# Kernel tuning notes

Hardware: AMD Instinct MI355X
Metric: run time of the kernel (lower is better)

## Reference

```python
import jax, jax.numpy as jnp
import numpy as np

NEG_SLOPE = 0.2  # negative_slope of LeakyReLU in GATConv
N_NODES = 50000
N_EDGES = 800000
R = 2
IN_DIM = 128
HID = 32
HEADS = 4
OUT = 32


def setup_inputs() -> dict:
    key = jax.random.key(0)
    ks = jax.random.split(key, 12)
    s = 0.1  # keep pre-activations tame
    x = jax.random.normal(ks[0], (N_NODES, IN_DIM), dtype=jnp.float32)
    W1 = jax.random.normal(ks[1], (R, IN_DIM, HEADS * HID), dtype=jnp.float32) * s
    al1 = jax.random.normal(ks[2], (R, HEADS, HID), dtype=jnp.float32) * s
    ar1 = jax.random.normal(ks[3], (R, HEADS, HID), dtype=jnp.float32) * s
    b1 = jax.random.normal(ks[4], (R, HEADS * HID), dtype=jnp.float32) * s
    W2 = jax.random.normal(ks[5], (R, HEADS * HID, HEADS * OUT), dtype=jnp.float32) * s
    al2 = jax.random.normal(ks[6], (R, HEADS, OUT), dtype=jnp.float32) * s
    ar2 = jax.random.normal(ks[7], (R, HEADS, OUT), dtype=jnp.float32) * s
    b2 = jax.random.normal(ks[8], (R, HEADS * OUT), dtype=jnp.float32) * s
    edges = jax.random.randint(ks[9], (R, 2, N_EDGES), 0, N_NODES, dtype=jnp.int32)
    return {"x": x, "W1": W1, "al1": al1, "ar1": ar1, "b1": b1,
            "W2": W2, "al2": al2, "ar2": ar2, "b2": b2, "edges": edges}


def _gat_rel(h, W, al, ar, src, dst, n):
    """Single-relation GATConv aggregation (no bias/residual/activation)."""
    H, D = al.shape
    feat = (h @ W).reshape(n, H, D)                   # [N,H,D]
    el = jnp.einsum('nhd,hd->nh', feat, al)           # [N,H]
    er = jnp.einsum('nhd,hd->nh', feat, ar)
    e = el[src] + er[dst]                             # [E,H]
    e = jnp.where(e > 0, e, NEG_SLOPE * e)            # LeakyReLU
    # edge softmax over incoming edges of each dst node (numerically stable)
    m = jax.ops.segment_max(e, dst, num_segments=n)
    ex = jnp.exp(e - m[dst])
    denom = jax.ops.segment_sum(ex, dst, num_segments=n)
    alpha = ex / jnp.maximum(denom[dst], 1e-9)        # [E,H]
    msg = alpha[:, :, None] * feat[src]               # [E,H,D]
    return jax.ops.segment_sum(msg, dst, num_segments=n)  # [N,H,D]


def reference(x, W1, al1, ar1, b1, W2, al2, ar2, b2, edges):
    n = x.shape[0]
    r_count = edges.shape[0]
    H1, D1 = al1.shape[1:]
    # --- layer 1: per-relation GATConv (bias + elu inside), sum across relations
    acc = jnp.zeros((n, H1, D1), dtype=x.dtype)
    for r in range(r_count):
        src, dst = edges[r, 0], edges[r, 1]
        o = _gat_rel(x, W1[r], al1[r], ar1[r], src, dst, n)
        acc = acc + jax.nn.elu(o + b1[r].reshape(1, H1, D1))
    h = acc.reshape(n, H1 * D1)                       # flatten heads
    # --- layer 2: residual (identity, since in == heads*out), bias, no activation
    H2, D2 = al2.shape[1:]
    res = h.reshape(n, H2, D2)
    acc2 = jnp.zeros((n, H2, D2), dtype=x.dtype)
    for r in range(r_count):
        src, dst = edges[r, 0], edges[r, 1]
        o = _gat_rel(h, W2[r], al2[r], ar2[r], src, dst, n)
        acc2 = acc2 + o + res + b2[r].reshape(1, H2, D2)
    return acc2.mean(axis=1)                          # mean over heads -> [N, OUT]
```

## Files before the change

### kernel.cpp

```cpp
#include <hip/hip_runtime.h>
#include <math.h>

#define HEADS 4
#define DIM 32
#define FDIM 128
#define EPB 8192
#define BPBSH 8
#define WB 16

typedef __attribute__((ext_vector_type(8))) short short8;
typedef __attribute__((ext_vector_type(16))) float float16;

__device__ __forceinline__ unsigned short f2bf(float x) {
  unsigned u = __float_as_uint(x);
  u += 0x7FFFu + ((u >> 16) & 1);
  return (unsigned short)(u >> 16);
}

__global__ __launch_bounds__(256) void binA_kernel(const int* __restrict__ edges,
    int* __restrict__ cntA, const float* __restrict__ W1, const float* __restrict__ W2,
    unsigned short* __restrict__ WT, int E, int BA, int BAp, int R) {
  int r = blockIdx.y, blk = blockIdx.x, t = threadIdx.x;
  if (blk >= BA) {
    int wb = blk - BA;
    int base = wb * (32768 / WB);
#pragma unroll
    for (int j = 0; j < 32768 / WB; j += 256) {
      int idx = base + j + t;
      int layer = idx >> 14;
      int rem = idx & 16383;
      int n = rem >> 7, k = rem & 127;
      const float* W = layer ? (W2 + (size_t)r * FDIM * FDIM)
                             : (W1 + (size_t)r * FDIM * FDIM);
      WT[((size_t)(layer * R + r) << 14) + rem] = f2bf(W[k * FDIM + n]);
    }
    return;
  }
  __shared__ int hist[256];
  hist[t] = 0;
  __syncthreads();
  const int* dst = edges + (size_t)r * 2 * E + E;
  int base = blk * EPB;
#pragma unroll
  for (int j = 0; j < EPB / 256; ++j) {
    int e = base + t + j * 256;
    if (e < E) atomicAdd(&hist[dst[e] >> BPBSH], 1);
  }
  __syncthreads();
  cntA[((size_t)r * 256 + t) * BAp + blk] = hist[t];
}

__global__ __launch_bounds__(256) void scanA_kernel(int* __restrict__ cntA,
    int* __restrict__ bucketBase, int E, int NB, int BA, int BAp) {
  __shared__ int stot[256];
  int r = blockIdx.x, b = threadIdx.x;
  int* row = cntA + ((size_t)r * 256 + b) * BAp;
  int tot = 0;
  if (b < NB)
    for (int blk = 0; blk < BA; ++blk) tot += row[blk];
  stot[b] = tot;
  __syncthreads();
  for (int ofs = 1; ofs < 256; ofs <<= 1) {
    int u = (b >= ofs) ? stot[b - ofs] : 0;
    __syncthreads();
    stot[b] += u;
    __syncthreads();
  }
  int excl = stot[b] - tot;
  if (b < NB) bucketBase[r * 257 + b] = excl;
  if (b == 0) bucketBase[r * 257 + NB] = E;
  if (b < NB) {
    int run = excl;
    for (int blk = 0; blk < BA; ++blk) {
      int c = row[blk];
      row[blk] = run;
      run += c;
    }
  }
}

__global__ __launch_bounds__(256) void scatterA_kernel(const int* __restrict__ edges,
    const int* __restrict__ cntA, unsigned* __restrict__ binned, int E, int BA, int BAp) {
  __shared__ int cur[256];
  int r = blockIdx.y, blk = blockIdx.x, t = threadIdx.x;
  cur[t] = cntA[((size_t)r * 256 + t) * BAp + blk];
  __syncthreads();
  const int* srcp = edges + (size_t)r * 2 * E;
  const int* dstp = srcp + E;
  unsigned* bout = binned + (size_t)r * E;
  int base = blk * EPB;
#pragma unroll
  for (int j = 0; j < EPB / 256; ++j) {
    int e = base + t + j * 256;
    if (e < E) {
      int d = dstp[e], s = srcp[e];
      int pos = atomicAdd(&cur[d >> BPBSH], 1);
      bout[pos] = ((unsigned)d << 16) | (unsigned)s;
    }
  }
}

__global__ __launch_bounds__(256) void passB_kernel(const unsigned* __restrict__ binned,
    const int* __restrict__ bucketBase, int* __restrict__ csr, int* __restrict__ indptr,
    int E, int N, int NB) {
  __shared__ int cnt[256];
  __shared__ int off[256];
  __shared__ int cur[256];
  int r = blockIdx.y, b = blockIdx.x, t = threadIdx.x;
  int beg = bucketBase[r * 257 + b];
  int end = bucketBase[r * 257 + b + 1];
  cnt[t] = 0;
  __syncthreads();
  const unsigned* bin = binned + (size_t)r * E;
  for (int i = beg + t; i < end; i += 256)
    atomicAdd(&cnt[(bin[i] >> 16) & 255], 1);
  __syncthreads();
  for (int ofs = 1; ofs < 256; ofs <<= 1) {
    int u = (t >= ofs) ? cnt[t - ofs] : 0;
    __syncthreads();
    cnt[t] += u;
    __syncthreads();
  }
  int ex = beg + ((t > 0) ? cnt[t - 1] : 0);
  off[t] = ex;
  cur[t] = ex;
  __syncthreads();
  int node = b * 256 + t;
  if (node < N) indptr[(size_t)r * (N + 1) + node] = off[t];
  if (b == NB - 1 && t == 0) indptr[(size_t)r * (N + 1) + N] = E;
  int* csr_r = csr + (size_t)r * E;
  for (int i = beg + t; i < end; i += 256) {
    unsigned p = bin[i];
    int rank = atomicAdd(&cur[(p >> 16) & 255], 1);
    csr_r[rank] = (int)(p & 0xFFFFu);
  }
}

__global__ __launch_bounds__(256) void mm_kernel(const float* __restrict__ A,
    const unsigned short* __restrict__ WTl, const float* __restrict__ al_all,
    const float* __restrict__ ar_all, unsigned short* __restrict__ featb_all,
    float* __restrict__ el_all, float* __restrict__ er_all, int N) {
  __shared__ unsigned short sA[128 * 136];
  __shared__ float sAl[FDIM], sAr[FDIM];
  int r = blockIdx.y;
  const unsigned short* WT = WTl + (size_t)r * FDIM * FDIM;
  int row0 = blockIdx.x * 128;
  int t = threadIdx.x;
  if (t < FDIM) {
    sAl[t] = al_all[r * FDIM + t];
    sAr[t] = ar_all[r * FDIM + t];
  }
#pragma unroll
  for (int it = 0; it < 16; ++it) {
    int idx = t * 4 + it * 1024;
    int row = idx >> 7, k = idx & 127;
    int grow = row0 + row;
    float4 v = make_float4(0.f, 0.f, 0.f, 0.f);
    if (grow < N) v = *(const float4*)(A + (size_t)grow * FDIM + k);
    unsigned short* p = sA + row * 136 + k;
    p[0] = f2bf(v.x); p[1] = f2bf(v.y); p[2] = f2bf(v.z); p[3] = f2bf(v.w);
  }
  __syncthreads();
  int lane = t & 63, w = t >> 6;
  int m = lane & 31, q = lane >> 5;
  float16 acc[4] = {0.f, 0.f, 0.f, 0.f};
#pragma unroll
  for (int kc = 0; kc < 8; ++kc) {
    int ko = kc * 16 + q * 8;
    short8 a = *(const short8*)(sA + (w * 32 + m) * 136 + ko);
#pragma unroll
    for (int nt = 0; nt < 4; ++nt) {
      short8 bb = *(const short8*)(WT + (size_t)(nt * 32 + m) * FDIM + ko);
      acc[nt] = __builtin_amdgcn_mfma_f32_32x32x16_bf16(a, bb, acc[nt], 0, 0, 0);
    }
  }
  __syncthreads();
#pragma unroll
  for (int nt = 0; nt < 4; ++nt) {
#pragma unroll
    for (int reg = 0; reg < 16; ++reg) {
      int rr = (reg & 3) + 8 * (reg >> 2) + 4 * q;
      sA[(w * 32 + rr) * 136 + nt * 32 + m] = f2bf(acc[nt][reg]);
    }
  }
  __syncthreads();
  unsigned short* fb = featb_all + (size_t)r * N * FDIM;
#pragma unroll
  for (int it = 0; it < 8; ++it) {
    int idx = (t + it * 256) * 8;
    int row = idx >> 7, k = idx & 127;
    int grow = row0 + row;
    if (grow < N)
      *(uint4*)(fb + (size_t)grow * FDIM + k) = *(const uint4*)(sA + row * 136 + k);
  }
  int rowc = t >> 1, grow = row0 + rowc;
  if (grow < N) {
    float* elr = el_all + (size_t)r * N * 4;
    float* err_ = er_all + (size_t)r * N * 4;
#pragma unroll
    for (int hh = 0; hh < 2; ++hh) {
      int hd = (t & 1) * 2 + hh;
      const uint4* rp4 = (const uint4*)(sA + rowc * 136 + hd * DIM);
      const float4* alp = (const float4*)(sAl + hd * DIM);
      const float4* arp = (const float4*)(sAr + hd * DIM);
      float sl = 0.f, sr = 0.f;
#pragma unroll
      for (int gq = 0; gq < 4; ++gq) {
        uint4 u = rp4[gq];
        float4 a0 = alp[2 * gq], a1 = alp[2 * gq + 1];
        float4 r0 = arp[2 * gq], r1 = arp[2 * gq + 1];
        unsigned uv[4] = {u.x, u.y, u.z, u.w};
        float fv[8];
#pragma unroll
        for (int j = 0; j < 4; ++j) {
          fv[2 * j] = __uint_as_float(uv[j] << 16);
          fv[2 * j + 1] = __uint_as_float(uv[j] & 0xFFFF0000u);
        }
        sl = fmaf(fv[0], a0.x, sl); sr = fmaf(fv[0], r0.x, sr);
        sl = fmaf(fv[1], a0.y, sl); sr = fmaf(fv[1], r0.y, sr);
        sl = fmaf(fv[2], a0.z, sl); sr = fmaf(fv[2], r0.z, sr);
        sl = fmaf(fv[3], a0.w, sl); sr = fmaf(fv[3], r0.w, sr);
        sl = fmaf(fv[4], a1.x, sl); sr = fmaf(fv[4], r1.x, sr);
        sl = fmaf(fv[5], a1.y, sl); sr = fmaf(fv[5], r1.y, sr);
        sl = fmaf(fv[6], a1.z, sl); sr = fmaf(fv[6], r1.z, sr);
        sl = fmaf(fv[7], a1.w, sl); sr = fmaf(fv[7], r1.w, sr);
      }
      elr[(size_t)grow * 4 + hd] = sl;
      err_[(size_t)grow * 4 + hd] = sr;
    }
  }
}

__global__ __launch_bounds__(256) void agg1_kernel(const unsigned short* __restrict__ featb,
    const float* __restrict__ el, const float* __restrict__ er,
    const int* __restrict__ indptr, const int* __restrict__ csr,
    const float* __restrict__ bias, float* __restrict__ hout, int N, int E, int R) {
  int t = blockIdx.x * 256 + threadIdx.x;
  int node = t >> 3;
  if (node >= N) return;
  int hd = t & 3, sub = (t >> 2) & 1;
  float tot[32];
#pragma unroll
  for (int i = 0; i < 32; ++i) tot[i] = 0.f;
  for (int r = 0; r < R; ++r) {
    const unsigned short* f = featb + (size_t)r * N * FDIM + hd * DIM;
    const float* elr = el + (size_t)r * N * 4;
    const int* csr_r = csr + (size_t)r * E;
    const int* ip = indptr + (size_t)r * (N + 1);
    float er_h = er[(size_t)r * N * 4 + node * 4 + hd];
    int beg = ip[node], end = ip[node + 1];
    float l = 0.f, a[32];
#pragma unroll
    for (int i = 0; i < 32; ++i) a[i] = 0.f;
    for (int i = beg + sub; i < end; i += 2) {
      int s = csr_r[i];
      float ee = elr[s * 4 + hd] + er_h;
      ee = ee > 0.f ? ee : 0.2f * ee;
      float p = __expf(ee);
      const uint4* fp = (const uint4*)(f + (size_t)s * FDIM);
      uint4 u0 = fp[0], u1 = fp[1], u2 = fp[2], u3 = fp[3];
      l += p;
      unsigned uu[16] = {u0.x, u0.y, u0.z, u0.w, u1.x, u1.y, u1.z, u1.w,
                         u2.x, u2.y, u2.z, u2.w, u3.x, u3.y, u3.z, u3.w};
#pragma unroll
      for (int j = 0; j < 16; ++j) {
        float f0 = __uint_as_float(uu[j] << 16);
        float f1 = __uint_as_float(uu[j] & 0xFFFF0000u);
        a[2 * j]     = fmaf(p, f0, a[2 * j]);
        a[2 * j + 1] = fmaf(p, f1, a[2 * j + 1]);
      }
    }
    l += __shfl_xor(l, 4);
#pragma unroll
    for (int i = 0; i < 32; ++i) a[i] += __shfl_xor(a[i], 4);
    float inv = (l > 0.f) ? 1.f / l : 0.f;
    const float4* b4 = (const float4*)(bias + r * FDIM + hd * DIM);
#pragma unroll
    for (int g = 0; g < 8; ++g) {
      float4 bv = b4[g];
      float v0 = a[4 * g] * inv + bv.x;
      float v1 = a[4 * g + 1] * inv + bv.y;
      float v2 = a[4 * g + 2] * inv + bv.z;
      float v3 = a[4 * g + 3] * inv + bv.w;
      tot[4 * g]     += v0 > 0.f ? v0 : __expf(v0) - 1.f;
      tot[4 * g + 1] += v1 > 0.f ? v1 : __expf(v1) - 1.f;
      tot[4 * g + 2] += v2 > 0.f ? v2 : __expf(v2) - 1.f;
      tot[4 * g + 3] += v3 > 0.f ? v3 : __expf(v3) - 1.f;
    }
  }
  if (sub == 0) {
    float4* hp = (float4*)(hout + (size_t)node * FDIM + hd * DIM);
#pragma unroll
    for (int g = 0; g < 8; ++g)
      hp[g] = make_float4(tot[4 * g], tot[4 * g + 1], tot[4 * g + 2], tot[4 * g + 3]);
  }
}

__global__ __launch_bounds__(256) void agg2_kernel(const unsigned short* __restrict__ featb,
    const float* __restrict__ el, const float* __restrict__ er,
    const int* __restrict__ indptr, const int* __restrict__ csr,
    const float* __restrict__ bias, const float* __restrict__ hf,
    float* __restrict__ out, int N, int E, int R) {
  int t = blockIdx.x * 256 + threadIdx.x;
  int node = t >> 3;
  if (node >= N) return;
  int hd = t & 3, sub = (t >> 2) & 1;
  float tot[32];
#pragma unroll
  for (int i = 0; i < 32; ++i) tot[i] = 0.f;
  for (int r = 0; r < R; ++r) {
    const unsigned short* f = featb + (size_t)r * N * FDIM + hd * DIM;
    const float* elr = el + (size_t)r * N * 4;
    const int* csr_r = csr + (size_t)r * E;
    const int* ip = indptr + (size_t)r * (N + 1);
    float er_h = er[(size_t)r * N * 4 + node * 4 + hd];
    int beg = ip[node], end = ip[node + 1];
    float l = 0.f, a[32];
#pragma unroll
    for (int i = 0; i < 32; ++i) a[i] = 0.f;
    for (int i = beg + sub; i < end; i += 2) {
      int s = csr_r[i];
      float ee = elr[s * 4 + hd] + er_h;
      ee = ee > 0.f ? ee : 0.2f * ee;
      float p = __expf(ee);
      const uint4* fp = (const uint4*)(f + (size_t)s * FDIM);
      uint4 u0 = fp[0], u1 = fp[1], u2 = fp[2], u3 = fp[3];
      l += p;
      unsigned uu[16] = {u0.x, u0.y, u0.z, u0.w, u1.x, u1.y, u1.z, u1.w,
                         u2.x, u2.y, u2.z, u2.w, u3.x, u3.y, u3.z, u3.w};
#pragma unroll
      for (int j = 0; j < 16; ++j) {
        float f0 = __uint_as_float(uu[j] << 16);
        float f1 = __uint_as_float(uu[j] & 0xFFFF0000u);
        a[2 * j]     = fmaf(p, f0, a[2 * j]);
        a[2 * j + 1] = fmaf(p, f1, a[2 * j + 1]);
      }
    }
    l += __shfl_xor(l, 4);
#pragma unroll
    for (int i = 0; i < 32; ++i) a[i] += __shfl_xor(a[i], 4);
    float inv = (l > 0.f) ? 1.f / l : 0.f;
    const float4* b4 = (const float4*)(bias + r * FDIM + hd * DIM);
#pragma unroll
    for (int g = 0; g < 8; ++g) {
      float4 bv = b4[g];
      tot[4 * g]     += a[4 * g] * inv + bv.x;
      tot[4 * g + 1] += a[4 * g + 1] * inv + bv.y;
      tot[4 * g + 2] += a[4 * g + 2] * inv + bv.z;
      tot[4 * g + 3] += a[4 * g + 3] * inv + bv.w;
    }
  }
  {
    const float4* rv4 = (const float4*)(hf + (size_t)node * FDIM + hd * DIM);
#pragma unroll
    for (int g = 0; g < 8; ++g) {
      float4 rv = rv4[g];
      tot[4 * g]     += R * rv.x;
      tot[4 * g + 1] += R * rv.y;
      tot[4 * g + 2] += R * rv.z;
      tot[4 * g + 3] += R * rv.w;
    }
  }
#pragma unroll
  for (int i = 0; i < 32; ++i) {
    float v = tot[i];
    v += __shfl_xor(v, 1);
    v += __shfl_xor(v, 2);
    tot[i] = v * 0.25f;
  }
  if (sub == 0) {
    float4* op = (float4*)(out + (size_t)node * 32 + hd * 8);
    op[0] = make_float4(tot[hd * 8], tot[hd * 8 + 1], tot[hd * 8 + 2], tot[hd * 8 + 3]);
    op[1] = make_float4(tot[hd * 8 + 4], tot[hd * 8 + 5], tot[hd * 8 + 6], tot[hd * 8 + 7]);
  }
}

extern "C" void kernel_launch(void* const* d_in, const int* in_sizes, int n_in,
                              void* d_out, int out_size, void* d_ws, size_t ws_size,
                              hipStream_t stream) {
  const float* x   = (const float*)d_in[0];
  const float* W1  = (const float*)d_in[1];
  const float* al1 = (const float*)d_in[2];
  const float* ar1 = (const float*)d_in[3];
  const float* b1  = (const float*)d_in[4];
  const float* W2  = (const float*)d_in[5];
  const float* al2 = (const float*)d_in[6];
  const float* ar2 = (const float*)d_in[7];
  const float* b2  = (const float*)d_in[8];
  const int* edges = (const int*)d_in[9];
  float* out = (float*)d_out;

  const int N = in_sizes[0] / FDIM;
  const int R = in_sizes[1] / (FDIM * FDIM);
  const int E = in_sizes[9] / (2 * R);
  const int BA = (E + EPB - 1) / EPB;
  const int BAp = (BA + 3) & ~3;
  const int NB = (N + 255) >> BPBSH;

  char* ws = (char*)d_ws;
  size_t off = 0;
  auto alloc = [&](size_t bytes) {
    char* p = ws + off;
    off += (bytes + 255) & ~(size_t)255;
    return p;
  };
  unsigned short* featb = (unsigned short*)alloc((size_t)R * N * FDIM * 2);
  unsigned short* WT    = (unsigned short*)alloc((size_t)2 * R * FDIM * FDIM * 2);
  float* el = (float*)alloc((size_t)R * N * 4 * 4);
  float* er = (float*)alloc((size_t)R * N * 4 * 4);
  float* h  = (float*)alloc((size_t)N * FDIM * 4);
  int* cntA = (int*)alloc((size_t)R * 256 * BAp * 4);
  int* bucketBase = (int*)alloc((size_t)R * 257 * 4);
  unsigned* binned = (unsigned*)alloc((size_t)R * E * 4);
  int* csr = (int*)alloc((size_t)R * E * 4);
  int* indptr = (int*)alloc((size_t)R * (N + 1) * 4);

  dim3 bgrid(BA + WB, R);
  binA_kernel<<<bgrid, 256, 0, stream>>>(edges, cntA, W1, W2, WT, E, BA, BAp, R);
  scanA_kernel<<<R, 256, 0, stream>>>(cntA, bucketBase, E, NB, BA, BAp);
  dim3 sgrid(BA, R);
  scatterA_kernel<<<sgrid, 256, 0, stream>>>(edges, cntA, binned, E, BA, BAp);
  dim3 pgrid(NB, R);
  passB_kernel<<<pgrid, 256, 0, stream>>>(binned, bucketBase, csr, indptr, E, N, NB);

  dim3 mmgrid((N + 127) / 128, R);
  int agrid = (N * 8 + 255) / 256;

  mm_kernel<<<mmgrid, 256, 0, stream>>>(x, WT, al1, ar1, featb, el, er, N);
  agg1_kernel<<<agrid, 256, 0, stream>>>(featb, el, er, indptr, csr, b1, h, N, E, R);

  mm_kernel<<<mmgrid, 256, 0, stream>>>(h, WT + (size_t)R * FDIM * FDIM, al2, ar2, featb, el, er, N);
  agg2_kernel<<<agrid, 256, 0, stream>>>(featb, el, er, indptr, csr, b2, h, out, N, E, R);
}
```

Before: 369.1 us.

## Split aggregation across relations per thread group and unroll edge loop by two

The aggregation kernels now give each node 16 threads instead of 8, so the two relations are processed in parallel by separate lane groups and summed with an extra cross-lane shuffle. The edge loop is unrolled to issue two neighbors' gathers before accumulating, and launch bounds request 4 blocks per CU. The aim is more memory-level parallelism for the latency-bound gathers. The cost is twice as many threads, extra shuffles, and possible register pressure from the doubled in-flight loads.

```diff
diff --git a/kernel.cpp b/kernel.cpp
--- a/kernel.cpp
+++ b/kernel.cpp
@@ -231,18 +231,31 @@
   }
 }
 
-__global__ __launch_bounds__(256) void agg1_kernel(const unsigned short* __restrict__ featb,
+__device__ __forceinline__ void acc_edge(float (&a)[32], uint4 u0, uint4 u1,
+                                         uint4 u2, uint4 u3, float p) {
+  unsigned uu[16] = {u0.x, u0.y, u0.z, u0.w, u1.x, u1.y, u1.z, u1.w,
+                     u2.x, u2.y, u2.z, u2.w, u3.x, u3.y, u3.z, u3.w};
+#pragma unroll
+  for (int j = 0; j < 16; ++j) {
+    float f0 = __uint_as_float(uu[j] << 16);
+    float f1 = __uint_as_float(uu[j] & 0xFFFF0000u);
+    a[2 * j]     = fmaf(p, f0, a[2 * j]);
+    a[2 * j + 1] = fmaf(p, f1, a[2 * j + 1]);
+  }
+}
+
+__global__ __launch_bounds__(256, 4) void agg1_kernel(const unsigned short* __restrict__ featb,
     const float* __restrict__ el, const float* __restrict__ er,
     const int* __restrict__ indptr, const int* __restrict__ csr,
     const float* __restrict__ bias, float* __restrict__ hout, int N, int E, int R) {
   int t = blockIdx.x * 256 + threadIdx.x;
-  int node = t >> 3;
+  int node = t >> 4;
   if (node >= N) return;
-  int hd = t & 3, sub = (t >> 2) & 1;
+  int hd = t & 3, rr = (t >> 2) & 1, sub = (t >> 3) & 1;
   float tot[32];
 #pragma unroll
   for (int i = 0; i < 32; ++i) tot[i] = 0.f;
-  for (int r = 0; r < R; ++r) {
+  for (int r = rr; r < R; r += 2) {
     const unsigned short* f = featb + (size_t)r * N * FDIM + hd * DIM;
     const float* elr = el + (size_t)r * N * 4;
     const int* csr_r = csr + (size_t)r * E;
@@ -252,27 +265,35 @@
     float l = 0.f, a[32];
 #pragma unroll
     for (int i = 0; i < 32; ++i) a[i] = 0.f;
-    for (int i = beg + sub; i < end; i += 2) {
+    int i = beg + sub;
+    for (; i + 2 < end; i += 4) {
+      int s0 = csr_r[i], s1 = csr_r[i + 2];
+      const uint4* fp0 = (const uint4*)(f + (size_t)s0 * FDIM);
+      const uint4* fp1 = (const uint4*)(f + (size_t)s1 * FDIM);
+      float ee0 = elr[s0 * 4 + hd];
+      float ee1 = elr[s1 * 4 + hd];
+      uint4 u00 = fp0[0], u01 = fp0[1], u02 = fp0[2], u03 = fp0[3];
+      uint4 u10 = fp1[0], u11 = fp1[1], u12 = fp1[2], u13 = fp1[3];
+      ee0 += er_h; ee0 = ee0 > 0.f ? ee0 : 0.2f * ee0;
+      ee1 += er_h; ee1 = ee1 > 0.f ? ee1 : 0.2f * ee1;
+      float p0 = __expf(ee0), p1 = __expf(ee1);
+      l += p0 + p1;
+      acc_edge(a, u00, u01, u02, u03, p0);
+      acc_edge(a, u10, u11, u12, u13, p1);
+    }
+    if (i < end) {
       int s = csr_r[i];
+      const uint4* fp = (const uint4*)(f + (size_t)s * FDIM);
       float ee = elr[s * 4 + hd] + er_h;
+      uint4 u0 = fp[0], u1 = fp[1], u2 = fp[2], u3 = fp[3];
       ee = ee > 0.f ? ee : 0.2f * ee;
       float p = __expf(ee);
-      const uint4* fp = (const uint4*)(f + (size_t)s * FDIM);
-      uint4 u0 = fp[0], u1 = fp[1], u2 = fp[2], u3 = fp[3];
       l += p;
-      unsigned uu[16] = {u0.x, u0.y, u0.z, u0.w, u1.x, u1.y, u1.z, u1.w,
-                         u2.x, u2.y, u2.z, u2.w, u3.x, u3.y, u3.z, u3.w};
-#pragma unroll
-      for (int j = 0; j < 16; ++j) {
-        float f0 = __uint_as_float(uu[j] << 16);
-        float f1 = __uint_as_float(uu[j] & 0xFFFF0000u);
-        a[2 * j]     = fmaf(p, f0, a[2 * j]);
-        a[2 * j + 1] = fmaf(p, f1, a[2 * j + 1]);
-      }
-    }
-    l += __shfl_xor(l, 4);
-#pragma unroll
-    for (int i = 0; i < 32; ++i) a[i] += __shfl_xor(a[i], 4);
+      acc_edge(a, u0, u1, u2, u3, p);
+    }
+    l += __shfl_xor(l, 8);
+#pragma unroll
+    for (int k = 0; k < 32; ++k) a[k] += __shfl_xor(a[k], 8);
     float inv = (l > 0.f) ? 1.f / l : 0.f;
     const float4* b4 = (const float4*)(bias + r * FDIM + hd * DIM);
 #pragma unroll
@@ -288,7 +309,9 @@
       tot[4 * g + 3] += v3 > 0.f ? v3 : __expf(v3) - 1.f;
     }
   }
-  if (sub == 0) {
+#pragma unroll
+  for (int k = 0; k < 32; ++k) tot[k] += __shfl_xor(tot[k], 4);
+  if ((t & 12) == 0) {
     float4* hp = (float4*)(hout + (size_t)node * FDIM + hd * DIM);
 #pragma unroll
     for (int g = 0; g < 8; ++g)
@@ -296,19 +319,19 @@
   }
 }
 
-__global__ __launch_bounds__(256) void agg2_kernel(const unsigned short* __restrict__ featb,
+__global__ __launch_bounds__(256, 4) void agg2_kernel(const unsigned short* __restrict__ featb,
     const float* __restrict__ el, const float* __restrict__ er,
     const int* __restrict__ indptr, const int* __restrict__ csr,
     const float* __restrict__ bias, const float* __restrict__ hf,
     float* __restrict__ out, int N, int E, int R) {
   int t = blockIdx.x * 256 + threadIdx.x;
-  int node = t >> 3;
+  int node = t >> 4;
   if (node >= N) return;
-  int hd = t & 3, sub = (t >> 2) & 1;
+  int hd = t & 3, rr = (t >> 2) & 1, sub = (t >> 3) & 1;
   float tot[32];
 #pragma unroll
   for (int i = 0; i < 32; ++i) tot[i] = 0.f;
-  for (int r = 0; r < R; ++r) {
+  for (int r = rr; r < R; r += 2) {
     const unsigned short* f = featb + (size_t)r * N * FDIM + hd * DIM;
     const float* elr = el + (size_t)r * N * 4;
     const int* csr_r = csr + (size_t)r * E;
@@ -318,27 +341,35 @@
     float l = 0.f, a[32];
 #pragma unroll
     for (int i = 0; i < 32; ++i) a[i] = 0.f;
-    for (int i = beg + sub; i < end; i += 2) {
+    int i = beg + sub;
+    for (; i + 2 < end; i += 4) {
+      int s0 = csr_r[i], s1 = csr_r[i + 2];
+      const uint4* fp0 = (const uint4*)(f + (size_t)s0 * FDIM);
+      const uint4* fp1 = (const uint4*)(f + (size_t)s1 * FDIM);
+      float ee0 = elr[s0 * 4 + hd];
+      float ee1 = elr[s1 * 4 + hd];
+      uint4 u00 = fp0[0], u01 = fp0[1], u02 = fp0[2], u03 = fp0[3];
+      uint4 u10 = fp1[0], u11 = fp1[1], u12 = fp1[2], u13 = fp1[3];
+      ee0 += er_h; ee0 = ee0 > 0.f ? ee0 : 0.2f * ee0;
+      ee1 += er_h; ee1 = ee1 > 0.f ? ee1 : 0.2f * ee1;
+      float p0 = __expf(ee0), p1 = __expf(ee1);
+      l += p0 + p1;
+      acc_edge(a, u00, u01, u02, u03, p0);
+      acc_edge(a, u10, u11, u12, u13, p1);
+    }
+    if (i < end) {
       int s = csr_r[i];
+      const uint4* fp = (const uint4*)(f + (size_t)s * FDIM);
       float ee = elr[s * 4 + hd] + er_h;
+      uint4 u0 = fp[0], u1 = fp[1], u2 = fp[2], u3 = fp[3];
       ee = ee > 0.f ? ee : 0.2f * ee;
       float p = __expf(ee);
-      const uint4* fp = (const uint4*)(f + (size_t)s * FDIM);
-      uint4 u0 = fp[0], u1 = fp[1], u2 = fp[2], u3 = fp[3];
       l += p;
-      unsigned uu[16] = {u0.x, u0.y, u0.z, u0.w, u1.x, u1.y, u1.z, u1.w,
-                         u2.x, u2.y, u2.z, u2.w, u3.x, u3.y, u3.z, u3.w};
-#pragma unroll
-      for (int j = 0; j < 16; ++j) {
-        float f0 = __uint_as_float(uu[j] << 16);
-        float f1 = __uint_as_float(uu[j] & 0xFFFF0000u);
-        a[2 * j]     = fmaf(p, f0, a[2 * j]);
-        a[2 * j + 1] = fmaf(p, f1, a[2 * j + 1]);
-      }
-    }
-    l += __shfl_xor(l, 4);
-#pragma unroll
-    for (int i = 0; i < 32; ++i) a[i] += __shfl_xor(a[i], 4);
+      acc_edge(a, u0, u1, u2, u3, p);
+    }
+    l += __shfl_xor(l, 8);
+#pragma unroll
+    for (int k = 0; k < 32; ++k) a[k] += __shfl_xor(a[k], 8);
     float inv = (l > 0.f) ? 1.f / l : 0.f;
     const float4* b4 = (const float4*)(bias + r * FDIM + hd * DIM);
 #pragma unroll
@@ -350,6 +381,8 @@
       tot[4 * g + 3] += a[4 * g + 3] * inv + bv.w;
     }
   }
+#pragma unroll
+  for (int k = 0; k < 32; ++k) tot[k] += __shfl_xor(tot[k], 4);
   {
     const float4* rv4 = (const float4*)(hf + (size_t)node * FDIM + hd * DIM);
 #pragma unroll
@@ -368,7 +401,7 @@
     v += __shfl_xor(v, 2);
     tot[i] = v * 0.25f;
   }
-  if (sub == 0) {
+  if ((t & 12) == 0) {
     float4* op = (float4*)(out + (size_t)node * 32 + hd * 8);
     op[0] = make_float4(tot[hd * 8], tot[hd * 8 + 1], tot[hd * 8 + 2], tot[hd * 8 + 3]);
     op[1] = make_float4(tot[hd * 8 + 4], tot[hd * 8 + 5], tot[hd * 8 + 6], tot[hd * 8 + 7]);
@@ -424,7 +457,7 @@
   passB_kernel<<<pgrid, 256, 0, stream>>>(binned, bucketBase, csr, indptr, E, N, NB);
 
   dim3 mmgrid((N + 127) / 128, R);
-  int agrid = (N * 8 + 255) / 256;
+  int agrid = (N * 16 + 255) / 256;
 
   mm_kernel<<<mmgrid, 256, 0, stream>>>(x, WT, al1, ar1, featb, el, er, N);
   agg1_kernel<<<agrid, 256, 0, stream>>>(featb, el, er, indptr, csr, b1, h, N, E, R);
```

Measured after the change: 439.7 us. 19.1% more time.

## Sort nodes by degree for aggregation load balance and shrink CSR to 16-bit

Applied to the files above, without the earlier changes.

Adds a counting sort of nodes by total in-degree, in descending order: a histogram, a scan and a scatter build a permutation. The aggregation kernels then walk nodes in that order, so wavefronts hold nodes of similar degree and do less divergent looping. The CSR source indices are also stored as 16-bit shorts instead of ints, halving the index traffic. The sort adds four small launches, and the output and feature accesses per wavefront become scattered rather than contiguous. The 16-bit indices rely on node ids fitting in 16 bits, which already held in the packed binning format.

```diff
diff --git a/kernel.cpp b/kernel.cpp
--- a/kernel.cpp
+++ b/kernel.cpp
@@ -101,8 +101,8 @@
 }
 
 __global__ __launch_bounds__(256) void passB_kernel(const unsigned* __restrict__ binned,
-    const int* __restrict__ bucketBase, int* __restrict__ csr, int* __restrict__ indptr,
-    int E, int N, int NB) {
+    const int* __restrict__ bucketBase, unsigned short* __restrict__ csr,
+    int* __restrict__ indptr, int E, int N, int NB) {
   __shared__ int cnt[256];
   __shared__ int off[256];
   __shared__ int cur[256];
@@ -128,12 +128,54 @@
   int node = b * 256 + t;
   if (node < N) indptr[(size_t)r * (N + 1) + node] = off[t];
   if (b == NB - 1 && t == 0) indptr[(size_t)r * (N + 1) + N] = E;
-  int* csr_r = csr + (size_t)r * E;
+  unsigned short* csr_r = csr + (size_t)r * E;
   for (int i = beg + t; i < end; i += 256) {
     unsigned p = bin[i];
     int rank = atomicAdd(&cur[(p >> 16) & 255], 1);
-    csr_r[rank] = (int)(p & 0xFFFFu);
-  }
+    csr_r[rank] = (unsigned short)(p & 0xFFFFu);
+  }
+}
+
+__global__ __launch_bounds__(256) void degZero_kernel(int* __restrict__ dhist) {
+  dhist[threadIdx.x] = 0;
+}
+
+__global__ __launch_bounds__(256) void degHist_kernel(const int* __restrict__ indptr,
+    int* __restrict__ dhist, int N, int R) {
+  int n = blockIdx.x * 256 + threadIdx.x;
+  if (n >= N) return;
+  int d = 0;
+  for (int r = 0; r < R; ++r)
+    d += indptr[(size_t)r * (N + 1) + n + 1] - indptr[(size_t)r * (N + 1) + n];
+  if (d > 255) d = 255;
+  atomicAdd(&dhist[d], 1);
+}
+
+__global__ __launch_bounds__(256) void degScan_kernel(const int* __restrict__ dhist,
+    int* __restrict__ dcur) {
+  __shared__ int s[256];
+  int t = threadIdx.x;
+  s[t] = dhist[255 - t];
+  __syncthreads();
+  for (int ofs = 1; ofs < 256; ofs <<= 1) {
+    int u = (t >= ofs) ? s[t - ofs] : 0;
+    __syncthreads();
+    s[t] += u;
+    __syncthreads();
+  }
+  dcur[255 - t] = s[t] - dhist[255 - t];
+}
+
+__global__ __launch_bounds__(256) void degScatter_kernel(const int* __restrict__ indptr,
+    int* __restrict__ dcur, int* __restrict__ perm, int N, int R) {
+  int n = blockIdx.x * 256 + threadIdx.x;
+  if (n >= N) return;
+  int d = 0;
+  for (int r = 0; r < R; ++r)
+    d += indptr[(size_t)r * (N + 1) + n + 1] - indptr[(size_t)r * (N + 1) + n];
+  if (d > 255) d = 255;
+  int pos = atomicAdd(&dcur[d], 1);
+  perm[pos] = n;
 }
 
 __global__ __launch_bounds__(256) void mm_kernel(const float* __restrict__ A,
@@ -233,11 +275,13 @@
 
 __global__ __launch_bounds__(256) void agg1_kernel(const unsigned short* __restrict__ featb,
     const float* __restrict__ el, const float* __restrict__ er,
-    const int* __restrict__ indptr, const int* __restrict__ csr,
+    const int* __restrict__ indptr, const unsigned short* __restrict__ csr,
+    const int* __restrict__ perm,
     const float* __restrict__ bias, float* __restrict__ hout, int N, int E, int R) {
   int t = blockIdx.x * 256 + threadIdx.x;
-  int node = t >> 3;
-  if (node >= N) return;
+  int ni = t >> 3;
+  if (ni >= N) return;
+  int node = perm[ni];
   int hd = t & 3, sub = (t >> 2) & 1;
   float tot[32];
 #pragma unroll
@@ -245,7 +289,7 @@
   for (int r = 0; r < R; ++r) {
     const unsigned short* f = featb + (size_t)r * N * FDIM + hd * DIM;
     const float* elr = el + (size_t)r * N * 4;
-    const int* csr_r = csr + (size_t)r * E;
+    const unsigned short* csr_r = csr + (size_t)r * E;
     const int* ip = indptr + (size_t)r * (N + 1);
     float er_h = er[(size_t)r * N * 4 + node * 4 + hd];
     int beg = ip[node], end = ip[node + 1];
@@ -298,12 +342,14 @@
 
 __global__ __launch_bounds__(256) void agg2_kernel(const unsigned short* __restrict__ featb,
     const float* __restrict__ el, const float* __restrict__ er,
-    const int* __restrict__ indptr, const int* __restrict__ csr,
+    const int* __restrict__ indptr, const unsigned short* __restrict__ csr,
+    const int* __restrict__ perm,
     const float* __restrict__ bias, const float* __restrict__ hf,
     float* __restrict__ out, int N, int E, int R) {
   int t = blockIdx.x * 256 + threadIdx.x;
-  int node = t >> 3;
-  if (node >= N) return;
+  int ni = t >> 3;
+  if (ni >= N) return;
+  int node = perm[ni];
   int hd = t & 3, sub = (t >> 2) & 1;
   float tot[32];
 #pragma unroll
@@ -311,7 +357,7 @@
   for (int r = 0; r < R; ++r) {
     const unsigned short* f = featb + (size_t)r * N * FDIM + hd * DIM;
     const float* elr = el + (size_t)r * N * 4;
-    const int* csr_r = csr + (size_t)r * E;
+    const unsigned short* csr_r = csr + (size_t)r * E;
     const int* ip = indptr + (size_t)r * (N + 1);
     float er_h = er[(size_t)r * N * 4 + node * 4 + hd];
     int beg = ip[node], end = ip[node + 1];
@@ -412,8 +458,11 @@
   int* cntA = (int*)alloc((size_t)R * 256 * BAp * 4);
   int* bucketBase = (int*)alloc((size_t)R * 257 * 4);
   unsigned* binned = (unsigned*)alloc((size_t)R * E * 4);
-  int* csr = (int*)alloc((size_t)R * E * 4);
+  unsigned short* csr = (unsigned short*)alloc((size_t)R * E * 2);
   int* indptr = (int*)alloc((size_t)R * (N + 1) * 4);
+  int* dhist = (int*)alloc(256 * 4);
+  int* dcur  = (int*)alloc(256 * 4);
+  int* perm  = (int*)alloc((size_t)N * 4);
 
   dim3 bgrid(BA + WB, R);
   binA_kernel<<<bgrid, 256, 0, stream>>>(edges, cntA, W1, W2, WT, E, BA, BAp, R);
@@ -423,12 +472,18 @@
   dim3 pgrid(NB, R);
   passB_kernel<<<pgrid, 256, 0, stream>>>(binned, bucketBase, csr, indptr, E, N, NB);
 
+  int ngrid = (N + 255) / 256;
+  degZero_kernel<<<1, 256, 0, stream>>>(dhist);
+  degHist_kernel<<<ngrid, 256, 0, stream>>>(indptr, dhist, N, R);
+  degScan_kernel<<<1, 256, 0, stream>>>(dhist, dcur);
+  degScatter_kernel<<<ngrid, 256, 0, stream>>>(indptr, dcur, perm, N, R);
+
   dim3 mmgrid((N + 127) / 128, R);
   int agrid = (N * 8 + 255) / 256;
 
   mm_kernel<<<mmgrid, 256, 0, stream>>>(x, WT, al1, ar1, featb, el, er, N);
-  agg1_kernel<<<agrid, 256, 0, stream>>>(featb, el, er, indptr, csr, b1, h, N, E, R);
+  agg1_kernel<<<agrid, 256, 0, stream>>>(featb, el, er, indptr, csr, perm, b1, h, N, E, R);
 
   mm_kernel<<<mmgrid, 256, 0, stream>>>(h, WT + (size_t)R * FDIM * FDIM, al2, ar2, featb, el, er, N);
-  agg2_kernel<<<agrid, 256, 0, stream>>>(featb, el, er, indptr, csr, b2, h, out, N, E, R);
-}
+  agg2_kernel<<<agrid, 256, 0, stream>>>(featb, el, er, indptr, csr, perm, b2, h, out, N, E, R);
+}
```

New measurement: 559.2 us. +51.5%, slower.
